# Kernel tuning notes

Hardware: AMD Instinct MI355X
Metric: run time of the kernel (lower is better)

The kernel has to match this reference:

```python
import jax, jax.numpy as jnp
import numpy as np

B, H, W, E = 4, 128, 128, 512
NH = 16
WH = WW = 8
DFF = 2048
EPS = 1e-5
N = WH * WW  # tokens per window
HD = E // NH  # head dim

# static relative-position index table: bias[q, k] = table[k_h - q_h + WH-1, k_w - q_w + WW-1]
_coords = np.stack(np.meshgrid(np.arange(WH), np.arange(WW), indexing='ij'), -1).reshape(-1, 2)  # (N, 2)
_rel = _coords[None, :, :] - _coords[:, None, :]  # (N, N, 2), key - query
_IDX_H = _rel[..., 0] + WH - 1
_IDX_W = _rel[..., 1] + WW - 1


def setup_inputs() -> dict:
    key = jax.random.key(0)
    ks = jax.random.split(key, 8)
    s = 0.02
    return {
        'x': jax.random.normal(ks[0], (B, H * W, E), jnp.float32),
        'in_proj_weight': jax.random.normal(ks[1], (3 * E, E), jnp.float32) * s,
        'in_proj_bias': jnp.zeros((3 * E,), jnp.float32),
        'out_proj_weight': jax.random.normal(ks[2], (E, E), jnp.float32) * s,
        'out_proj_bias': jnp.zeros((E,), jnp.float32),
        'pos_emb': jax.random.normal(ks[3], (2 * WH - 1, 2 * WW - 1, 1), jnp.float32) * s,
        'lin1_w': jax.random.normal(ks[4], (DFF, E), jnp.float32) * s,
        'lin1_b': jnp.zeros((DFF,), jnp.float32),
        'lin2_w': jax.random.normal(ks[5], (E, DFF), jnp.float32) * s,
        'lin2_b': jnp.zeros((E,), jnp.float32),
        'ln1_w': jnp.ones((E,), jnp.float32),
        'ln1_b': jnp.zeros((E,), jnp.float32),
        'ln2_w': jnp.ones((E,), jnp.float32),
        'ln2_b': jnp.zeros((E,), jnp.float32),
    }


def _layer_norm(y, g, b):
    m = y.mean(-1, keepdims=True)
    v = y.var(-1, keepdims=True)
    return (y - m) * jax.lax.rsqrt(v + EPS) * g + b


def _forward(x, in_proj_weight, in_proj_bias, out_proj_weight, out_proj_bias,
             pos_emb, lin1_w, lin1_b, lin2_w, lin2_b, ln1_w, ln1_b, ln2_w, ln2_b):
    # relative positional bias shared across heads: (1, N, N)
    bias = pos_emb[_IDX_H, _IDX_W, :].transpose(2, 0, 1)

    def attn(y):
        # window partition: (B, H*W, E) -> (B*nWin, N, E)
        yw = y.reshape(B, H // WH, WH, W // WW, WW, E)
        yw = yw.transpose(0, 1, 3, 2, 4, 5).reshape(-1, N, E)
        qw, kw, vw = jnp.split(in_proj_weight, 3, axis=0)
        qb, kb, vb = jnp.split(in_proj_bias, 3, axis=0)
        q = (yw @ qw.T + qb).reshape(-1, N, NH, HD).transpose(0, 2, 1, 3)  # (Bw, h, N, d)
        k = (yw @ kw.T + kb).reshape(-1, N, NH, HD).transpose(0, 2, 1, 3)
        v = (yw @ vw.T + vb).reshape(-1, N, NH, HD).transpose(0, 2, 1, 3)
        scores = jnp.einsum('bhqd,bhkd->bhqk', q, k) / np.sqrt(HD).astype(np.float32)
        scores = scores + bias[None]  # broadcast over windows and heads
        a = jax.nn.softmax(scores, axis=-1)
        o = jnp.einsum('bhqk,bhkd->bhqd', a, v)
        o = o.transpose(0, 2, 1, 3).reshape(-1, N, E)
        o = o @ out_proj_weight.T + out_proj_bias
        # reverse window partition
        o = o.reshape(B, H // WH, W // WW, WH, WW, E)
        return o.transpose(0, 1, 3, 2, 4, 5).reshape(B, H * W, E)

    # post-norm (norm_first=False): x = norm1(x + SA(x)); x = norm2(x + FF(x))
    z = _layer_norm(x + attn(x), ln1_w, ln1_b)
    ff = jax.nn.relu(z @ lin1_w.T + lin1_b) @ lin2_w.T + lin2_b
    return _layer_norm(z + ff, ln2_w, ln2_b)


def reference(x, in_proj_weight, in_proj_bias, out_proj_weight, out_proj_bias,
              pos_emb, lin1_w, lin1_b, lin2_w, lin2_b, ln1_w, ln1_b, ln2_w, ln2_b):
    return _forward(x, in_proj_weight, in_proj_bias, out_proj_weight, out_proj_bias,
                    pos_emb, lin1_w, lin1_b, lin2_w, lin2_b, ln1_w, ln1_b, ln2_w, ln2_b)
```

## Files before the change

### kernel.cpp

```cpp
#include <hip/hip_runtime.h>
#include <hip/hip_bf16.h>

#define NTOK   65536
#define E_     512
#define NH_    16
#define HD_    32
#define DFF_   2048
#define N3E    1536
#define MC     16384
#define NCHUNK 4

typedef __attribute__((ext_vector_type(8))) short short8;
typedef __attribute__((ext_vector_type(4))) short short4t;
typedef __attribute__((ext_vector_type(4))) float floatx4;

__device__ inline float b2f(short u) {
    union { float f; unsigned int i; } x;
    x.i = ((unsigned int)(unsigned short)u) << 16;
    return x.f;
}
__device__ inline short f2bs(float f) {
    __hip_bfloat16 h = __float2bfloat16(f);
    return *reinterpret_cast<short*>(&h);
}

__global__ __launch_bounds__(256) void cvt_kernel(const float* __restrict__ in,
                                                  __hip_bfloat16* __restrict__ out, int n) {
    int i = (blockIdx.x * 256 + threadIdx.x) * 8;
    if (i >= n) return;
    if (i + 7 < n) {
        float4 a = *(const float4*)(in + i);
        float4 b = *(const float4*)(in + i + 4);
        short8 o;
        o[0] = f2bs(a.x); o[1] = f2bs(a.y); o[2] = f2bs(a.z); o[3] = f2bs(a.w);
        o[4] = f2bs(b.x); o[5] = f2bs(b.y); o[6] = f2bs(b.z); o[7] = f2bs(b.w);
        *(short8*)(out + i) = o;
    } else {
        for (int u = i; u < n; ++u) out[u] = __float2bfloat16(in[u]);
    }
}

template<int EPI>
__global__ __launch_bounds__(256) void gemm_kernel(
    const __hip_bfloat16* __restrict__ A,
    const __hip_bfloat16* __restrict__ Bw,
    const float* __restrict__ bias,
    const void* __restrict__ res,
    void* __restrict__ out,
    int M, int N, int K)
{
    __shared__ __hip_bfloat16 As[128 * 32];
    __shared__ __hip_bfloat16 Bs[128 * 32];

    const int tid  = threadIdx.x;
    const int wave = tid >> 6;
    const int lane = tid & 63;
    const int tileN = blockIdx.x * 128;
    const int tileM = blockIdx.y * 128;

    const int wm = (wave >> 1) * 64;
    const int wn = (wave & 1) * 64;

    const int sRow  = lane >> 2;
    const int sColE = (lane & 3) * 8;

    floatx4 acc[4][4];
    #pragma unroll
    for (int i = 0; i < 4; ++i)
        #pragma unroll
        for (int j = 0; j < 4; ++j)
            acc[i][j] = (floatx4){0.f, 0.f, 0.f, 0.f};

    const int lm  = lane & 15;
    const int lkE = (lane >> 4) * 8;

    for (int k0 = 0; k0 < K; k0 += 32) {
        #pragma unroll
        for (int q = 0; q < 2; ++q) {
            const int chunk = wave * 2 + q;
            const int row   = chunk * 16 + sRow;
            const __hip_bfloat16* gA = A  + (size_t)(tileM + row) * K + k0 + sColE;
            const __hip_bfloat16* gB = Bw + (size_t)(tileN + row) * K + k0 + sColE;
            __builtin_amdgcn_global_load_lds((const __attribute__((address_space(1))) void*)gA,
                                             (__attribute__((address_space(3))) void*)(As + chunk * 512),
                                             16, 0, 0);
            __builtin_amdgcn_global_load_lds((const __attribute__((address_space(1))) void*)gB,
                                             (__attribute__((address_space(3))) void*)(Bs + chunk * 512),
                                             16, 0, 0);
        }
        __syncthreads();

        short8 af[4], bfr[4];
        #pragma unroll
        for (int i = 0; i < 4; ++i)
            af[i] = *(const short8*)(As + (wm + i * 16 + lm) * 32 + lkE);
        #pragma unroll
        for (int j = 0; j < 4; ++j)
            bfr[j] = *(const short8*)(Bs + (wn + j * 16 + lm) * 32 + lkE);

        #pragma unroll
        for (int i = 0; i < 4; ++i)
            #pragma unroll
            for (int j = 0; j < 4; ++j)
                acc[i][j] = __builtin_amdgcn_mfma_f32_16x16x32_bf16(af[i], bfr[j], acc[i][j], 0, 0, 0);
        __syncthreads();
    }

    const int rbase = (lane >> 4) * 4;
    #pragma unroll
    for (int i = 0; i < 4; ++i) {
        const int rl = wm + i * 16 + rbase;
        #pragma unroll
        for (int j = 0; j < 4; ++j) {
            const int n = tileN + wn + j * 16 + lm;
            const float bv = bias[n];
            #pragma unroll
            for (int r = 0; r < 4; ++r) {
                const int m = tileM + rl + r;
                const size_t idx = (size_t)m * N + n;
                float v = acc[i][j][r] + bv;
                if (EPI == 0) {
                    ((__hip_bfloat16*)out)[idx] = __float2bfloat16(v);
                } else if (EPI == 1) {
                    v += ((const float*)res)[idx];
                    ((float*)out)[idx] = v;
                } else if (EPI == 2) {
                    v = v > 0.f ? v : 0.f;
                    ((__hip_bfloat16*)out)[idx] = __float2bfloat16(v);
                } else {
                    v += __bfloat162float(((const __hip_bfloat16*)res)[idx]);
                    ((float*)out)[idx] = v;
                }
            }
        }
    }
}

__global__ __launch_bounds__(64) void attn_kernel(
    const __hip_bfloat16* __restrict__ qkv,
    const float* __restrict__ pos,
    __hip_bfloat16* __restrict__ obuf)
{
    __shared__ __align__(16) short vt[32][72];
    __shared__ __align__(16) short pl[64][72];
    __shared__ float ps[232];

    const int win = blockIdx.x;
    const int h   = blockIdx.y;
    const int l   = threadIdx.x;
    const int l15 = l & 15;
    const int g   = l >> 4;
    const int g8  = g * 8;

    const int base0 = (win >> 4) * 1024 + (win & 15) * 8;

    for (int u = l; u < 225; u += 64) ps[u] = pos[u];

    const int tok_l = base0 + (l >> 3) * 128 + (l & 7);
    const short8* vp = (const short8*)(qkv + (size_t)tok_l * N3E + 1024 + h * HD_);
    #pragma unroll
    for (int u = 0; u < 4; ++u) {
        short8 vv = vp[u];
        #pragma unroll
        for (int e = 0; e < 8; ++e) vt[u * 8 + e][l] = vv[e];
    }

    const int tokbase = base0 + (l15 >> 3) * 128 + (l15 & 7);
    short8 qf[4], kf[4];
    #pragma unroll
    for (int j = 0; j < 4; ++j) {
        const size_t tb = (size_t)(tokbase + 256 * j) * N3E + h * HD_ + g8;
        qf[j] = *(const short8*)(qkv + tb);
        kf[j] = *(const short8*)(qkv + tb + 512);
    }
    __syncthreads();

    floatx4 st[4][4];
    #pragma unroll
    for (int i = 0; i < 4; ++i)
        #pragma unroll
        for (int j = 0; j < 4; ++j)
            st[i][j] = __builtin_amdgcn_mfma_f32_16x16x32_bf16(
                kf[i], qf[j], (floatx4){0.f, 0.f, 0.f, 0.f}, 0, 0, 0);

    const float scale = 0.17677669529663687f;
    int kb[4];
    #pragma unroll
    for (int r = 0; r < 4; ++r) {
        const int qq = g * 4 + r;
        kb[r] = (qq >> 3) * 15 + (qq & 7);
    }

    #pragma unroll
    for (int j = 0; j < 4; ++j) {
        const int q   = j * 16 + l15;
        const int qoi = 112 - (q >> 3) * 15 - (q & 7);
        float p[16];
        float mx = -1e30f;
        #pragma unroll
        for (int i = 0; i < 4; ++i)
            #pragma unroll
            for (int r = 0; r < 4; ++r) {
                const float sv = st[i][j][r] * scale + ps[30 * i + kb[r] + qoi];
                p[i * 4 + r] = sv;
                mx = fmaxf(mx, sv);
            }
        mx = fmaxf(mx, __shfl_xor(mx, 16));
        mx = fmaxf(mx, __shfl_xor(mx, 32));
        float sum = 0.f;
        #pragma unroll
        for (int u = 0; u < 16; ++u) { p[u] = __expf(p[u] - mx); sum += p[u]; }
        sum += __shfl_xor(sum, 16);
        sum += __shfl_xor(sum, 32);
        const float inv = 1.f / sum;
        #pragma unroll
        for (int i = 0; i < 4; ++i) {
            short4t pk;
            #pragma unroll
            for (int r = 0; r < 4; ++r) pk[r] = f2bs(p[i * 4 + r] * inv);
            *(short4t*)&pl[q][i * 16 + g * 4] = pk;
        }
    }
    __syncthreads();

    short8 vb[2][2];
    #pragma unroll
    for (int nt = 0; nt < 2; ++nt)
        #pragma unroll
        for (int kk = 0; kk < 2; ++kk)
            vb[nt][kk] = *(const short8*)&vt[nt * 16 + l15][kk * 32 + g8];

    floatx4 o[4][2];
    #pragma unroll
    for (int j = 0; j < 4; ++j)
        #pragma unroll
        for (int nt = 0; nt < 2; ++nt)
            o[j][nt] = (floatx4){0.f, 0.f, 0.f, 0.f};

    #pragma unroll
    for (int j = 0; j < 4; ++j) {
        #pragma unroll
        for (int kk = 0; kk < 2; ++kk) {
            const short8 pa = *(const short8*)&pl[j * 16 + l15][kk * 32 + g8];
            #pragma unroll
            for (int nt = 0; nt < 2; ++nt)
                o[j][nt] = __builtin_amdgcn_mfma_f32_16x16x32_bf16(
                    pa, vb[nt][kk], o[j][nt], 0, 0, 0);
        }
    }

    #pragma unroll
    for (int r = 0; r < 4; ++r) {
        const int qq = g * 4 + r;
        const int tb = base0 + (qq >> 3) * 128 + (qq & 7);
        #pragma unroll
        for (int j = 0; j < 4; ++j) {
            __hip_bfloat16* op = obuf + (size_t)(tb + 256 * j) * E_ + h * HD_ + l15;
            op[0]  = __float2bfloat16(o[j][0][r]);
            op[16] = __float2bfloat16(o[j][1][r]);
        }
    }
}

template<int OUTMODE>
__global__ __launch_bounds__(256) void ln_kernel(
    const float* __restrict__ in, const float* __restrict__ gw,
    const float* __restrict__ gb, void* __restrict__ out)
{
    const int row  = blockIdx.x * 4 + (threadIdx.x >> 6);
    const int lane = threadIdx.x & 63;
    const float* rp = in + (size_t)row * 512 + lane * 8;
    float4 v0 = *(const float4*)rp;
    float4 v1 = *(const float4*)(rp + 4);
    float s  = v0.x + v0.y + v0.z + v0.w + v1.x + v1.y + v1.z + v1.w;
    float sq = v0.x * v0.x + v0.y * v0.y + v0.z * v0.z + v0.w * v0.w
             + v1.x * v1.x + v1.y * v1.y + v1.z * v1.z + v1.w * v1.w;
    #pragma unroll
    for (int off = 32; off > 0; off >>= 1) {
        s  += __shfl_xor(s, off);
        sq += __shfl_xor(sq, off);
    }
    const float mean = s * (1.f / 512.f);
    const float var  = sq * (1.f / 512.f) - mean * mean;
    const float rstd = rsqrtf(var + 1e-5f);
    const int c = lane * 8;
    float4 g0 = *(const float4*)(gw + c), g1 = *(const float4*)(gw + c + 4);
    float4 b0 = *(const float4*)(gb + c), b1 = *(const float4*)(gb + c + 4);
    float r[8];
    r[0] = (v0.x - mean) * rstd * g0.x + b0.x;
    r[1] = (v0.y - mean) * rstd * g0.y + b0.y;
    r[2] = (v0.z - mean) * rstd * g0.z + b0.z;
    r[3] = (v0.w - mean) * rstd * g0.w + b0.w;
    r[4] = (v1.x - mean) * rstd * g1.x + b1.x;
    r[5] = (v1.y - mean) * rstd * g1.y + b1.y;
    r[6] = (v1.z - mean) * rstd * g1.z + b1.z;
    r[7] = (v1.w - mean) * rstd * g1.w + b1.w;
    if (OUTMODE == 0) {
        short8 o;
        #pragma unroll
        for (int e = 0; e < 8; ++e) o[e] = f2bs(r[e]);
        *(short8*)((__hip_bfloat16*)out + (size_t)row * 512 + c) = o;
    } else {
        float* po = (float*)out + (size_t)row * 512 + c;
        *(float4*)po       = make_float4(r[0], r[1], r[2], r[3]);
        *(float4*)(po + 4) = make_float4(r[4], r[5], r[6], r[7]);
    }
}

static const size_t OFF_WQKV = 0;
static const size_t OFF_WOUT = 1572864;
static const size_t OFF_W1   = 2097152;
static const size_t OFF_W2   = 4194304;
static const size_t OFF_XB   = 6291456;
static const size_t OFF_ZB   = 73400320;
static const size_t OFF_QKVC = 140509184;
static const size_t OFF_OBUFC= 190840832;
static const size_t OFF_H1C  = OFF_QKVC;

extern "C" void kernel_launch(void* const* d_in, const int* in_sizes, int n_in,
                              void* d_out, int out_size, void* d_ws, size_t ws_size,
                              hipStream_t stream) {
    (void)in_sizes; (void)n_in; (void)out_size; (void)ws_size;
    const float* x    = (const float*)d_in[0];
    const float* wqkv = (const float*)d_in[1];
    const float* bqkv = (const float*)d_in[2];
    const float* wout = (const float*)d_in[3];
    const float* bout = (const float*)d_in[4];
    const float* pos  = (const float*)d_in[5];
    const float* w1   = (const float*)d_in[6];
    const float* b1   = (const float*)d_in[7];
    const float* w2   = (const float*)d_in[8];
    const float* b2   = (const float*)d_in[9];
    const float* g1   = (const float*)d_in[10];
    const float* bb1  = (const float*)d_in[11];
    const float* g2   = (const float*)d_in[12];
    const float* bb2  = (const float*)d_in[13];
    float* outp = (float*)d_out;

    char* ws = (char*)d_ws;
    __hip_bfloat16* wqkv_b = (__hip_bfloat16*)(ws + OFF_WQKV);
    __hip_bfloat16* wout_b = (__hip_bfloat16*)(ws + OFF_WOUT);
    __hip_bfloat16* w1_b   = (__hip_bfloat16*)(ws + OFF_W1);
    __hip_bfloat16* w2_b   = (__hip_bfloat16*)(ws + OFF_W2);
    __hip_bfloat16* xb     = (__hip_bfloat16*)(ws + OFF_XB);
    __hip_bfloat16* zb     = (__hip_bfloat16*)(ws + OFF_ZB);
    __hip_bfloat16* qkvc   = (__hip_bfloat16*)(ws + OFF_QKVC);
    __hip_bfloat16* obufc  = (__hip_bfloat16*)(ws + OFF_OBUFC);
    __hip_bfloat16* h1c    = (__hip_bfloat16*)(ws + OFF_H1C);

    {
        int n;
        n = N3E * E_;    cvt_kernel<<<(n / 8 + 255) / 256, 256, 0, stream>>>(wqkv, wqkv_b, n);
        n = E_ * E_;     cvt_kernel<<<(n / 8 + 255) / 256, 256, 0, stream>>>(wout, wout_b, n);
        n = DFF_ * E_;   cvt_kernel<<<(n / 8 + 255) / 256, 256, 0, stream>>>(w1, w1_b, n);
        n = E_ * DFF_;   cvt_kernel<<<(n / 8 + 255) / 256, 256, 0, stream>>>(w2, w2_b, n);
        n = NTOK * E_;   cvt_kernel<<<(n / 8 + 255) / 256, 256, 0, stream>>>(x, xb, n);
    }

    for (int c = 0; c < NCHUNK; ++c) {
        const size_t tok0 = (size_t)c * MC;
        gemm_kernel<0><<<dim3(N3E / 128, MC / 128), 256, 0, stream>>>(
            xb + tok0 * E_, wqkv_b, bqkv, nullptr, qkvc, MC, N3E, E_);
        attn_kernel<<<dim3(256, NH_), 64, 0, stream>>>(qkvc, pos, obufc);
        gemm_kernel<1><<<dim3(E_ / 128, MC / 128), 256, 0, stream>>>(
            obufc, wout_b, bout, x + tok0 * E_, outp + tok0 * E_, MC, E_, E_);
    }

    ln_kernel<0><<<NTOK / 4, 256, 0, stream>>>(outp, g1, bb1, zb);

    for (int c = 0; c < NCHUNK; ++c) {
        const size_t tok0 = (size_t)c * MC;
        gemm_kernel<2><<<dim3(DFF_ / 128, MC / 128), 256, 0, stream>>>(
            zb + tok0 * E_, w1_b, b1, nullptr, h1c, MC, DFF_, E_);
        gemm_kernel<3><<<dim3(E_ / 128, MC / 128), 256, 0, stream>>>(
            h1c, w2_b, b2, zb + tok0 * E_, outp + tok0 * E_, MC, E_, DFF_);
    }

    ln_kernel<1><<<NTOK / 4, 256, 0, stream>>>(outp, g2, bb2, outp);
}
```

Measured before the change: 1.160 ms.

## Rewrite GEMM with double-buffered LDS, 128x256 tiles, swizzle and 8 waves

Replaces the single-buffered 128x128 GEMM with a 512-thread kernel that computes 128x256 tiles. It uses a K step of 64, double-buffers LDS loads with explicit vmcnt waits, applies an XOR swizzle to avoid LDS bank conflicts, and raises wave priority around the MFMA blocks. The intent is to overlap global-to-LDS transfers with MFMA work, cut barrier count, and raise operand reuse. The cost is 96 KB of LDS per block, which lowers occupancy, and fewer blocks for the N=512 GEMMs.

```diff
diff --git a/kernel.cpp b/kernel.cpp
--- a/kernel.cpp
+++ b/kernel.cpp
@@ -41,7 +41,7 @@
 }
 
 template<int EPI>
-__global__ __launch_bounds__(256) void gemm_kernel(
+__global__ __launch_bounds__(512) void gemm2_kernel(
     const __hip_bfloat16* __restrict__ A,
     const __hip_bfloat16* __restrict__ Bw,
     const float* __restrict__ bias,
@@ -49,20 +49,25 @@
     void* __restrict__ out,
     int M, int N, int K)
 {
-    __shared__ __hip_bfloat16 As[128 * 32];
-    __shared__ __hip_bfloat16 Bs[128 * 32];
+    __shared__ __align__(16) short As[2][128 * 64];
+    __shared__ __align__(16) short Bs[2][256 * 64];
 
     const int tid  = threadIdx.x;
-    const int wave = tid >> 6;
+    const int wid  = tid >> 6;
     const int lane = tid & 63;
-    const int tileN = blockIdx.x * 128;
+    const int tileN = blockIdx.x * 256;
     const int tileM = blockIdx.y * 128;
 
-    const int wm = (wave >> 1) * 64;
-    const int wn = (wave & 1) * 64;
-
-    const int sRow  = lane >> 2;
-    const int sColE = (lane & 3) * 8;
+    const int wm = (wid >> 2) * 64;
+    const int wn = (wid & 3) * 64;
+    const int lm = lane & 15;
+    const int g  = lane >> 4;
+
+    const int lr = lane >> 3;
+    const int ss = (lane & 7) ^ lr;
+
+    const __hip_bfloat16* gA = A  + (size_t)(tileM + wid * 16 + lr) * K + ss * 8;
+    const __hip_bfloat16* gB = Bw + (size_t)(tileN + wid * 32 + lr) * K + ss * 8;
 
     floatx4 acc[4][4];
     #pragma unroll
@@ -71,42 +76,69 @@
         for (int j = 0; j < 4; ++j)
             acc[i][j] = (floatx4){0.f, 0.f, 0.f, 0.f};
 
-    const int lm  = lane & 15;
-    const int lkE = (lane >> 4) * 8;
-
-    for (int k0 = 0; k0 < K; k0 += 32) {
-        #pragma unroll
-        for (int q = 0; q < 2; ++q) {
-            const int chunk = wave * 2 + q;
-            const int row   = chunk * 16 + sRow;
-            const __hip_bfloat16* gA = A  + (size_t)(tileM + row) * K + k0 + sColE;
-            const __hip_bfloat16* gB = Bw + (size_t)(tileN + row) * K + k0 + sColE;
-            __builtin_amdgcn_global_load_lds((const __attribute__((address_space(1))) void*)gA,
-                                             (__attribute__((address_space(3))) void*)(As + chunk * 512),
-                                             16, 0, 0);
-            __builtin_amdgcn_global_load_lds((const __attribute__((address_space(1))) void*)gB,
-                                             (__attribute__((address_space(3))) void*)(Bs + chunk * 512),
-                                             16, 0, 0);
-        }
-        __syncthreads();
-
-        short8 af[4], bfr[4];
-        #pragma unroll
-        for (int i = 0; i < 4; ++i)
-            af[i] = *(const short8*)(As + (wm + i * 16 + lm) * 32 + lkE);
-        #pragma unroll
-        for (int j = 0; j < 4; ++j)
-            bfr[j] = *(const short8*)(Bs + (wn + j * 16 + lm) * 32 + lkE);
-
-        #pragma unroll
-        for (int i = 0; i < 4; ++i)
+#define STAGE2(b, k0)                                                                     \
+    {                                                                                     \
+        _Pragma("unroll")                                                                 \
+        for (int q = 0; q < 2; ++q)                                                       \
+            __builtin_amdgcn_global_load_lds(                                             \
+                (const __attribute__((address_space(1))) void*)(gA + (size_t)(q * 8) * K + (k0)), \
+                (__attribute__((address_space(3))) void*)(&As[b][(wid * 2 + q) * 512]),   \
+                16, 0, 0);                                                                \
+        _Pragma("unroll")                                                                 \
+        for (int q = 0; q < 4; ++q)                                                       \
+            __builtin_amdgcn_global_load_lds(                                             \
+                (const __attribute__((address_space(1))) void*)(gB + (size_t)(q * 8) * K + (k0)), \
+                (__attribute__((address_space(3))) void*)(&Bs[b][(wid * 4 + q) * 512]),   \
+                16, 0, 0);                                                                \
+    }
+
+    const int NT = K >> 6;
+
+    STAGE2(0, 0)
+    STAGE2(1, 64)
+    asm volatile("s_waitcnt vmcnt(6)\ns_barrier" ::: "memory");
+
+    const int lsw = (lm & 7);
+
+    for (int t = 0; t < NT; ++t) {
+        const int b = t & 1;
+        const short* pa = As[b];
+        const short* pb = Bs[b];
+
+        #pragma unroll
+        for (int ks = 0; ks < 2; ++ks) {
+            short8 af[4], bfr[4];
+            const int cs = ks * 4 + g;
+            const int so = (cs ^ lsw) * 8;
+            #pragma unroll
+            for (int i = 0; i < 4; ++i)
+                af[i] = *(const short8*)(pa + (wm + i * 16 + lm) * 64 + so);
             #pragma unroll
             for (int j = 0; j < 4; ++j)
-                acc[i][j] = __builtin_amdgcn_mfma_f32_16x16x32_bf16(af[i], bfr[j], acc[i][j], 0, 0, 0);
-        __syncthreads();
-    }
-
-    const int rbase = (lane >> 4) * 4;
+                bfr[j] = *(const short8*)(pb + (wn + j * 16 + lm) * 64 + so);
+
+            __builtin_amdgcn_s_setprio(1);
+            #pragma unroll
+            for (int i = 0; i < 4; ++i)
+                #pragma unroll
+                for (int j = 0; j < 4; ++j)
+                    acc[i][j] = __builtin_amdgcn_mfma_f32_16x16x32_bf16(af[i], bfr[j], acc[i][j], 0, 0, 0);
+            __builtin_amdgcn_s_setprio(0);
+        }
+
+        if (t + 1 < NT) {
+            asm volatile("s_waitcnt lgkmcnt(0)\ns_barrier" ::: "memory");
+            if (t + 2 < NT) {
+                STAGE2(b, (t + 2) * 64)
+                asm volatile("s_waitcnt vmcnt(6)\ns_barrier" ::: "memory");
+            } else {
+                asm volatile("s_waitcnt vmcnt(0)\ns_barrier" ::: "memory");
+            }
+        }
+    }
+#undef STAGE2
+
+    const int rbase = g * 4;
     #pragma unroll
     for (int i = 0; i < 4; ++i) {
         const int rl = wm + i * 16 + rbase;
@@ -359,10 +391,10 @@
 
     for (int c = 0; c < NCHUNK; ++c) {
         const size_t tok0 = (size_t)c * MC;
-        gemm_kernel<0><<<dim3(N3E / 128, MC / 128), 256, 0, stream>>>(
+        gemm2_kernel<0><<<dim3(N3E / 256, MC / 128), 512, 0, stream>>>(
             xb + tok0 * E_, wqkv_b, bqkv, nullptr, qkvc, MC, N3E, E_);
         attn_kernel<<<dim3(256, NH_), 64, 0, stream>>>(qkvc, pos, obufc);
-        gemm_kernel<1><<<dim3(E_ / 128, MC / 128), 256, 0, stream>>>(
+        gemm2_kernel<1><<<dim3(E_ / 256, MC / 128), 512, 0, stream>>>(
             obufc, wout_b, bout, x + tok0 * E_, outp + tok0 * E_, MC, E_, E_);
     }
 
@@ -370,9 +402,9 @@
 
     for (int c = 0; c < NCHUNK; ++c) {
         const size_t tok0 = (size_t)c * MC;
-        gemm_kernel<2><<<dim3(DFF_ / 128, MC / 128), 256, 0, stream>>>(
+        gemm2_kernel<2><<<dim3(DFF_ / 256, MC / 128), 512, 0, stream>>>(
             zb + tok0 * E_, w1_b, b1, nullptr, h1c, MC, DFF_, E_);
-        gemm_kernel<3><<<dim3(E_ / 128, MC / 128), 256, 0, stream>>>(
+        gemm2_kernel<3><<<dim3(E_ / 256, MC / 128), 512, 0, stream>>>(
             h1c, w2_b, b2, zb + tok0 * E_, outp + tok0 * E_, MC, E_, DFF_);
     }
 
```

New measurement: 1.169 ms. No clear change (+0.8%).
